# Optimization experiments

Hardware: AMD Instinct MI355X
Metric: run time of the kernel (lower is better)

Reference implementation:

```python
import jax, jax.numpy as jnp
import numpy as np

EMBED_DIM = 2048
NUM_HEADS = 16
NUM_KV_HEADS = 4
KEY_DIM = EMBED_DIM // NUM_HEADS  # 128
B, S = 2, 2048


def setup_inputs() -> dict:
    key = jax.random.key(0)
    ks = jax.random.split(key, 8)
    kv_dim = KEY_DIM * NUM_KV_HEADS
    sc_in = 1.0 / np.sqrt(EMBED_DIM)
    return {
        "query": jax.random.normal(ks[0], (B, S, EMBED_DIM), jnp.float32),
        "key": jax.random.normal(ks[1], (B, S, EMBED_DIM), jnp.float32),
        "value": jax.random.normal(ks[2], (B, S, EMBED_DIM), jnp.float32),
        "mask": jnp.ones((B, S), jnp.float32),
        "Wq": jax.random.normal(ks[3], (EMBED_DIM, EMBED_DIM), jnp.float32) * sc_in,
        "Wk": jax.random.normal(ks[4], (EMBED_DIM, kv_dim), jnp.float32) * sc_in,
        "Wv": jax.random.normal(ks[5], (EMBED_DIM, kv_dim), jnp.float32) * sc_in,
        "Wo": jax.random.normal(ks[6], (EMBED_DIM, EMBED_DIM), jnp.float32) * sc_in,
    }


def reference(query, key, value, mask, Wq, Wk, Wv, Wo):
    b, sq, _ = query.shape
    skv = key.shape[1]
    scale = 1.0 / float(KEY_DIM) ** 0.5
    # projections (no bias)
    q = (query @ Wq).reshape(b, sq, NUM_HEADS, KEY_DIM).transpose(0, 2, 1, 3)      # [B,H,Sq,D]
    k = (key @ Wk).reshape(b, skv, NUM_KV_HEADS, KEY_DIM).transpose(0, 2, 1, 3)    # [B,Hkv,Skv,D]
    v = (value @ Wv).reshape(b, skv, NUM_KV_HEADS, KEY_DIM).transpose(0, 2, 1, 3)  # [B,Hkv,Skv,D]
    n_rep = NUM_HEADS // NUM_KV_HEADS
    k_rep = jnp.repeat(k, n_rep, axis=1)  # [B,H,Skv,D]
    v_rep = jnp.repeat(v, n_rep, axis=1)  # [B,H,Skv,D]
    scores = jnp.einsum("bhqd,bhkd->bhqk", q, k_rep) * scale  # [B,H,Sq,Skv]
    scores = scores + (1.0 - mask[:, None, None, :].astype(scores.dtype)) * -1e9
    attn = jax.nn.softmax(scores, axis=-1)
    out = jnp.einsum("bhqk,bhkd->bhqd", attn, v_rep)  # [B,H,Sq,D]
    out = out.transpose(0, 2, 1, 3).reshape(b, sq, EMBED_DIM)
    return out @ Wo
```

## Files before the change

### kernel.cpp

```cpp
#include <hip/hip_runtime.h>
#include <hip/hip_bf16.h>

#define B_    2
#define S_    2048
#define E_    2048
#define H_    16
#define HKV_  4
#define D_    128
#define NTOK  4096
#define KVDIM 512

typedef __bf16 bf16x8 __attribute__((ext_vector_type(8)));
typedef __bf16 bf16x4 __attribute__((ext_vector_type(4)));
typedef float  f32x4  __attribute__((ext_vector_type(4)));

__device__ __forceinline__ void async_copy16(const void* g, void* l) {
  __builtin_amdgcn_global_load_lds(
      (const __attribute__((address_space(1))) unsigned int*)g,
      (__attribute__((address_space(3))) unsigned int*)l, 16, 0, 0);
}

__global__ __launch_bounds__(256) void transpose_all(
    const float* __restrict__ Wq, const float* __restrict__ Wk,
    const float* __restrict__ Wv, const float* __restrict__ Wo,
    __bf16* __restrict__ WTq, __bf16* __restrict__ WTk,
    __bf16* __restrict__ WTv, __bf16* __restrict__ WoT) {
  const float* in;
  __bf16* out;
  int C;
  switch (blockIdx.z) {
    case 0:  in = Wq; out = WTq; C = E_;   break;
    case 1:  in = Wk; out = WTk; C = KVDIM; break;
    case 2:  in = Wv; out = WTv; C = KVDIM; break;
    default: in = Wo; out = WoT; C = E_;   break;
  }
  const int c0 = blockIdx.x * 32;
  if (c0 >= C) return;
  const int r0 = blockIdx.y * 32;
  __shared__ float t[32][33];
  const int tr = threadIdx.x >> 3;
  const int tc = (threadIdx.x & 7) * 4;
  const float* ip = in + (size_t)(r0 + tr) * C + c0 + tc;
#pragma unroll
  for (int i = 0; i < 4; ++i) t[tr][tc + i] = ip[i];
  __syncthreads();
  __bf16* op = out + (size_t)(c0 + tr) * E_ + r0 + tc;
#pragma unroll
  for (int i = 0; i < 4; ++i) op[i] = (__bf16)t[tc + i][tr];
}

__global__ __launch_bounds__(256) void convert_q(const float* __restrict__ in,
                                                 __bf16* __restrict__ ob) {
  const size_t i = ((size_t)blockIdx.x * 256 + threadIdx.x) * 8;
  const f32x4 a0 = *(const f32x4*)(in + i);
  const f32x4 a1 = *(const f32x4*)(in + i + 4);
  bf16x8 v;
#pragma unroll
  for (int j = 0; j < 4; ++j) { v[j] = (__bf16)a0[j]; v[4 + j] = (__bf16)a1[j]; }
  *(bf16x8*)(ob + i) = v;
}

__global__ __launch_bounds__(512, 1) void gemm_pipe(
    const __bf16* __restrict__ A, const __bf16* __restrict__ Bt,
    float* __restrict__ Cf, __bf16* __restrict__ Cb, int M, int N, int K,
    int epi) {
  __shared__ __align__(16) __bf16 lds[2 * 24576];

  const int n0 = blockIdx.x * 256;
  const int m0 = blockIdx.y * 128;
  const int tid = threadIdx.x;
  const int w = tid >> 6;
  const int lane = tid & 63;
  const int quad = lane >> 4;
  const int l16 = lane & 15;
  const int wm = w >> 2;
  const int wn = w & 3;
  const int lr = lane >> 3;
  const int ls = lane & 7;

  const __bf16* pa[2];
  const __bf16* pb[4];
#pragma unroll
  for (int r = 0; r < 2; ++r) {
    const int row = r * 64 + w * 8 + lr;
    pa[r] = A + (size_t)(m0 + row) * K + ((ls ^ (row & 7)) * 8);
  }
#pragma unroll
  for (int r = 0; r < 4; ++r) {
    const int row = r * 64 + w * 8 + lr;
    pb[r] = Bt + (size_t)(n0 + row) * K + ((ls ^ (row & 7)) * 8);
  }

  auto stageA = [&](int bufi) {
    __bf16* base = lds + bufi * 24576;
#pragma unroll
    for (int r = 0; r < 2; ++r) {
      async_copy16(pa[r], base + (size_t)(r * 64 + w * 8) * 64);
      pa[r] += 64;
    }
  };
  auto stageB = [&](int bufi) {
    __bf16* base = lds + bufi * 24576 + 8192;
#pragma unroll
    for (int r = 0; r < 4; ++r) {
      async_copy16(pb[r], base + (size_t)(r * 64 + w * 8) * 64);
      pb[r] += 64;
    }
  };

  f32x4 acc[4][4] = {};
  const int NT = K >> 6;
  const int xr = l16 & 7;

  stageA(0);
  stageB(0);
  stageB(1);
  asm volatile("s_waitcnt vmcnt(4)" ::: "memory");
  __builtin_amdgcn_s_barrier();

  for (int t = 0; t < NT; ++t) {
    const __bf16* lA = lds + (t & 1) * 24576;
    const __bf16* lB = lA + 8192;

    bf16x8 af[2][2], bfr[4][2];
#pragma unroll
    for (int f = 0; f < 2; ++f) {
      const int rowb = (wm * 64 + f * 16 + l16) * 64;
#pragma unroll
      for (int ks = 0; ks < 2; ++ks)
        af[f][ks] = *(const bf16x8*)&lA[rowb + (((ks * 4 + quad) ^ xr) * 8)];
    }
#pragma unroll
    for (int g = 0; g < 4; ++g) {
      const int rowb = (wn * 64 + g * 16 + l16) * 64;
#pragma unroll
      for (int ks = 0; ks < 2; ++ks)
        bfr[g][ks] = *(const bf16x8*)&lB[rowb + (((ks * 4 + quad) ^ xr) * 8)];
    }
    if (t + 1 < NT) stageA((t + 1) & 1);
    __builtin_amdgcn_s_barrier();
    asm volatile("s_waitcnt lgkmcnt(0)" ::: "memory");
    __builtin_amdgcn_sched_barrier(0);
    __builtin_amdgcn_s_setprio(1);
#pragma unroll
    for (int f = 0; f < 2; ++f)
#pragma unroll
      for (int g = 0; g < 4; ++g) {
        acc[f][g] = __builtin_amdgcn_mfma_f32_16x16x32_bf16(af[f][0], bfr[g][0],
                                                            acc[f][g], 0, 0, 0);
        acc[f][g] = __builtin_amdgcn_mfma_f32_16x16x32_bf16(af[f][1], bfr[g][1],
                                                            acc[f][g], 0, 0, 0);
      }
    __builtin_amdgcn_s_setprio(0);
    __builtin_amdgcn_s_barrier();

    bf16x8 ah[2][2];
#pragma unroll
    for (int f = 0; f < 2; ++f) {
      const int rowb = (wm * 64 + (f + 2) * 16 + l16) * 64;
#pragma unroll
      for (int ks = 0; ks < 2; ++ks)
        ah[f][ks] = *(const bf16x8*)&lA[rowb + (((ks * 4 + quad) ^ xr) * 8)];
    }
    if (t + 2 < NT) stageB(t & 1);
    __builtin_amdgcn_s_barrier();
    asm volatile("s_waitcnt lgkmcnt(0)" ::: "memory");
    __builtin_amdgcn_sched_barrier(0);
    __builtin_amdgcn_s_setprio(1);
#pragma unroll
    for (int f = 0; f < 2; ++f)
#pragma unroll
      for (int g = 0; g < 4; ++g) {
        acc[f + 2][g] = __builtin_amdgcn_mfma_f32_16x16x32_bf16(
            ah[f][0], bfr[g][0], acc[f + 2][g], 0, 0, 0);
        acc[f + 2][g] = __builtin_amdgcn_mfma_f32_16x16x32_bf16(
            ah[f][1], bfr[g][1], acc[f + 2][g], 0, 0, 0);
      }
    __builtin_amdgcn_s_setprio(0);

    if (t + 2 < NT) {
      asm volatile("s_waitcnt vmcnt(4)" ::: "memory");
      __builtin_amdgcn_s_barrier();
    } else if (t + 1 < NT) {
      asm volatile("s_waitcnt vmcnt(0)" ::: "memory");
      __builtin_amdgcn_s_barrier();
    }
  }

#pragma unroll
  for (int f = 0; f < 4; ++f) {
#pragma unroll
    for (int g = 0; g < 4; ++g) {
#pragma unroll
      for (int r = 0; r < 4; ++r) {
        const int m = m0 + wm * 64 + f * 16 + quad * 4 + r;
        const int n = n0 + wn * 64 + g * 16 + l16;
        if (epi == 0) Cf[(size_t)m * N + n] = acc[f][g][r];
        else          Cb[(size_t)m * N + n] = (__bf16)acc[f][g][r];
      }
    }
  }
}

__global__ __launch_bounds__(256, 2) void gemm_kv(
    const float* __restrict__ key, const float* __restrict__ value,
    const __bf16* __restrict__ WTk, const __bf16* __restrict__ WTv,
    __bf16* __restrict__ Kp, __bf16* __restrict__ Vt) {
  __shared__ __align__(16) __bf16 As[128 * 32];
  __shared__ __align__(16) __bf16 Bs[128 * 32];

  const int bx = blockIdx.x;
  const float* A;
  const __bf16* Bt;
  int n0, epi;
  if (bx < 4) { A = key;   Bt = WTk; n0 = bx * 128;       epi = 0; }
  else        { A = value; Bt = WTv; n0 = (bx - 4) * 128; epi = 1; }
  const int m0 = blockIdx.y * 128;
  const int K = E_;
  const int N = KVDIM;

  const int tid = threadIdx.x;
  const int w = tid >> 6;
  const int lane = tid & 63;
  const int quad = lane >> 4;
  const int l16 = lane & 15;
  const int wr = w >> 1, wc = w & 1;
  const int brow = lane >> 2;
  const int bcol = (lane & 3) * 8;
  const int arow = lane >> 2;
  const int acol = (lane & 3) * 8;

  f32x4 acc[4][4] = {};

  for (int k0 = 0; k0 < K; k0 += 32) {
    __syncthreads();
#pragma unroll
    for (int c = 0; c < 2; ++c) {
      const int chunk = w * 2 + c;
      const int row = chunk * 16 + brow;
      async_copy16(Bt + (size_t)(n0 + row) * K + k0 + bcol, &Bs[chunk * 512]);
    }
#pragma unroll
    for (int s = 0; s < 2; ++s) {
      const int row = w * 32 + s * 16 + arow;
      const float* src = A + (size_t)(m0 + row) * K + k0 + acol;
      const f32x4 a0 = *(const f32x4*)src;
      const f32x4 a1 = *(const f32x4*)(src + 4);
      bf16x8 v;
#pragma unroll
      for (int j = 0; j < 4; ++j) { v[j] = (__bf16)a0[j]; v[4 + j] = (__bf16)a1[j]; }
      *(bf16x8*)&As[row * 32 + acol] = v;
    }
    __syncthreads();
    bf16x8 af[4], bfr[4];
#pragma unroll
    for (int i = 0; i < 4; ++i)
      af[i] = *(const bf16x8*)&As[(wr * 64 + i * 16 + l16) * 32 + quad * 8];
#pragma unroll
    for (int j = 0; j < 4; ++j)
      bfr[j] = *(const bf16x8*)&Bs[(wc * 64 + j * 16 + l16) * 32 + quad * 8];
#pragma unroll
    for (int i = 0; i < 4; ++i)
#pragma unroll
      for (int j = 0; j < 4; ++j)
        acc[i][j] = __builtin_amdgcn_mfma_f32_16x16x32_bf16(af[i], bfr[j],
                                                            acc[i][j], 0, 0, 0);
  }

#pragma unroll
  for (int i = 0; i < 4; ++i) {
#pragma unroll
    for (int j = 0; j < 4; ++j) {
#pragma unroll
      for (int r = 0; r < 4; ++r) {
        const int m = m0 + wr * 64 + i * 16 + quad * 4 + r;
        const int n = n0 + wc * 64 + j * 16 + l16;
        if (epi == 0) {
          Kp[(size_t)m * N + n] = (__bf16)acc[i][j][r];
        } else {
          const int b = m >> 11, s = m & (S_ - 1);
          Vt[((size_t)((b * HKV_ + (n >> 7)) * D_ + (n & (D_ - 1)))) * S_ + s] =
              (__bf16)acc[i][j][r];
        }
      }
    }
  }
}

__global__ __launch_bounds__(256, 2) void attn_kernel(
    const __bf16* __restrict__ Q, const __bf16* __restrict__ Kp,
    const __bf16* __restrict__ Vt, const float* __restrict__ mask,
    __bf16* __restrict__ Oa) {
  __shared__ __align__(16) __bf16 K_lds[64][136];
  __shared__ __align__(16) __bf16 V_lds[128][72];
  __shared__ __align__(16) __bf16 P_lds[4][32][72];

  const int tid = threadIdx.x;
  const int w = tid >> 6, lane = tid & 63, quad = lane >> 4, l16 = lane & 15;
  const int bh = blockIdx.y;
  const int b = bh >> 4, h = bh & 15, hkv = h >> 2;
  const int q0 = blockIdx.x * 128 + w * 32;

  const __bf16* qbase = Q + (size_t)(b * S_ + q0) * E_ + h * D_;
  bf16x8 qf[2][4];
#pragma unroll
  for (int m = 0; m < 2; ++m)
#pragma unroll
    for (int ks = 0; ks < 4; ++ks)
      qf[m][ks] = *(const bf16x8*)(qbase + (size_t)(m * 16 + l16) * E_ +
                                   ks * 32 + quad * 8);

  const __bf16* kbase = Kp + (size_t)(b * S_) * KVDIM + hkv * D_;
  const __bf16* vbase = Vt + (size_t)((b * HKV_ + hkv) * D_) * S_;
  const float* mbase = mask + b * S_;

  f32x4 o[2][8] = {};
  f32x4 lsum[2] = {};
  const float scale = 0.08838834764831845f;

  for (int kt = 0; kt < S_; kt += 64) {
    __syncthreads();
#pragma unroll
    for (int i = 0; i < 4; ++i) {
      const int r = w * 16 + i * 4 + (lane >> 4);
      bf16x8 kv = *(const bf16x8*)(kbase + (size_t)(kt + r) * KVDIM +
                                   (lane & 15) * 8);
      *(bf16x8*)&K_lds[r][(lane & 15) * 8] = kv;
    }
#pragma unroll
    for (int i = 0; i < 4; ++i) {
      const int r = w * 32 + i * 8 + (lane >> 3);
      bf16x8 vv = *(const bf16x8*)(vbase + (size_t)r * S_ + kt +
                                   (lane & 7) * 8);
      *(bf16x8*)&V_lds[r][(lane & 7) * 8] = vv;
    }
    __syncthreads();

    f32x4 s[2][4] = {};
    __builtin_amdgcn_s_setprio(1);
#pragma unroll
    for (int ks = 0; ks < 4; ++ks) {
#pragma unroll
      for (int n = 0; n < 4; ++n) {
        bf16x8 kf = *(const bf16x8*)&K_lds[n * 16 + l16][ks * 32 + quad * 8];
        s[0][n] = __builtin_amdgcn_mfma_f32_16x16x32_bf16(qf[0][ks], kf,
                                                          s[0][n], 0, 0, 0);
        s[1][n] = __builtin_amdgcn_mfma_f32_16x16x32_bf16(qf[1][ks], kf,
                                                          s[1][n], 0, 0, 0);
      }
    }
    __builtin_amdgcn_s_setprio(0);

    float bias[4];
#pragma unroll
    for (int n = 0; n < 4; ++n)
      bias[n] = (1.0f - mbase[kt + n * 16 + l16]) * -1e9f;
#pragma unroll
    for (int m = 0; m < 2; ++m) {
#pragma unroll
      for (int n = 0; n < 4; ++n) {
#pragma unroll
        for (int r = 0; r < 4; ++r) {
          const float p = __expf(s[m][n][r] * scale + bias[n]);
          lsum[m][r] += p;
          P_lds[w][m * 16 + quad * 4 + r][n * 16 + l16] = (__bf16)p;
        }
      }
    }

    __builtin_amdgcn_s_setprio(1);
#pragma unroll
    for (int ks2 = 0; ks2 < 2; ++ks2) {
      bf16x8 pa[2];
#pragma unroll
      for (int m = 0; m < 2; ++m)
        pa[m] = *(const bf16x8*)&P_lds[w][m * 16 + l16][ks2 * 32 + quad * 8];
#pragma unroll
      for (int dt = 0; dt < 8; ++dt) {
        bf16x8 vf = *(const bf16x8*)&V_lds[dt * 16 + l16][ks2 * 32 + quad * 8];
        o[0][dt] = __builtin_amdgcn_mfma_f32_16x16x32_bf16(pa[0], vf,
                                                           o[0][dt], 0, 0, 0);
        o[1][dt] = __builtin_amdgcn_mfma_f32_16x16x32_bf16(pa[1], vf,
                                                           o[1][dt], 0, 0, 0);
      }
    }
    __builtin_amdgcn_s_setprio(0);
  }

  __bf16* obase = Oa + (size_t)(b * S_ + q0) * E_ + h * D_;
#pragma unroll
  for (int m = 0; m < 2; ++m) {
#pragma unroll
    for (int r = 0; r < 4; ++r) {
      float v = lsum[m][r];
#pragma unroll
      for (int off = 1; off < 16; off <<= 1) v += __shfl_xor(v, off);
      const float inv = 1.0f / v;
#pragma unroll
      for (int dt = 0; dt < 8; ++dt)
        obase[(size_t)(m * 16 + quad * 4 + r) * E_ + dt * 16 + l16] =
            (__bf16)(o[m][dt][r] * inv);
    }
  }
}

extern "C" void kernel_launch(void* const* d_in, const int* in_sizes, int n_in,
                              void* d_out, int out_size, void* d_ws,
                              size_t ws_size, hipStream_t stream) {
  const float* query = (const float*)d_in[0];
  const float* key   = (const float*)d_in[1];
  const float* value = (const float*)d_in[2];
  const float* mask  = (const float*)d_in[3];
  const float* Wq    = (const float*)d_in[4];
  const float* Wk    = (const float*)d_in[5];
  const float* Wv    = (const float*)d_in[6];
  const float* Wo    = (const float*)d_in[7];
  float* out = (float*)d_out;

  __bf16* ws   = (__bf16*)d_ws;
  __bf16* Qp   = ws;
  __bf16* Kp   = Qp + (size_t)NTOK * E_;
  __bf16* Vt   = Kp + (size_t)NTOK * KVDIM;
  __bf16* WoT  = Vt + (size_t)NTOK * KVDIM;
  __bf16* WTq  = WoT + (size_t)E_ * E_;
  __bf16* WTk  = WTq + (size_t)E_ * E_;
  __bf16* WTv  = WTk + (size_t)KVDIM * E_;
  __bf16* Attn = WTq;
  __bf16* qb   = (__bf16*)d_out;

  transpose_all<<<dim3(64, 64, 4), 256, 0, stream>>>(Wq, Wk, Wv, Wo,
                                                     WTq, WTk, WTv, WoT);
  convert_q<<<dim3(4096), 256, 0, stream>>>(query, qb);
  gemm_kv<<<dim3(8, 32), 256, 0, stream>>>(key, value, WTk, WTv, Kp, Vt);
  gemm_pipe<<<dim3(E_ / 256, NTOK / 128), 512, 0, stream>>>(
      qb, WTq, nullptr, Qp, NTOK, E_, E_, 1);
  attn_kernel<<<dim3(S_ / 128, B_ * H_), 256, 0, stream>>>(Qp, Kp, Vt, mask,
                                                           Attn);
  gemm_pipe<<<dim3(E_ / 256, NTOK / 128), 512, 0, stream>>>(
      Attn, WoT, out, nullptr, NTOK, E_, E_, 0);
}
```

Before: 411.2 us.

## Fuse query conversion into transpose, swizzle GEMM tiles, keep attention P in registers

Query fp32-to-bf16 conversion now runs as an extra z-slice of the weight transpose kernel, which drops one launch, and the transpose uses wider 64-row tiles with vectorized loads and stores. The projection GEMM remaps block indices with a swizzle to improve L2 reuse across tiles. The attention kernel computes S transposed (K as the A operand), turns the probabilities into the PV operand layout with lane shuffles instead of a round trip through LDS, loads the mask bias as vectors, and raises occupancy to 3 blocks per SM. The risks are more shuffle instructions and higher register pressure under the tighter launch bound.

```diff
diff --git a/kernel.cpp b/kernel.cpp
--- a/kernel.cpp
+++ b/kernel.cpp
@@ -24,7 +24,25 @@
     const float* __restrict__ Wq, const float* __restrict__ Wk,
     const float* __restrict__ Wv, const float* __restrict__ Wo,
     __bf16* __restrict__ WTq, __bf16* __restrict__ WTk,
-    __bf16* __restrict__ WTv, __bf16* __restrict__ WoT) {
+    __bf16* __restrict__ WTv, __bf16* __restrict__ WoT,
+    const float* __restrict__ query, __bf16* __restrict__ qb) {
+  if (blockIdx.z == 4) {
+    const size_t i =
+        (((size_t)blockIdx.y * 64 + blockIdx.x) * 256 + threadIdx.x) * 16;
+    const f32x4 a0 = *(const f32x4*)(query + i);
+    const f32x4 a1 = *(const f32x4*)(query + i + 4);
+    const f32x4 a2 = *(const f32x4*)(query + i + 8);
+    const f32x4 a3 = *(const f32x4*)(query + i + 12);
+    bf16x8 v0, v1;
+#pragma unroll
+    for (int j = 0; j < 4; ++j) {
+      v0[j] = (__bf16)a0[j]; v0[4 + j] = (__bf16)a1[j];
+      v1[j] = (__bf16)a2[j]; v1[4 + j] = (__bf16)a3[j];
+    }
+    *(bf16x8*)(qb + i) = v0;
+    *(bf16x8*)(qb + i + 8) = v1;
+    return;
+  }
   const float* in;
   __bf16* out;
   int C;
@@ -36,28 +54,24 @@
   }
   const int c0 = blockIdx.x * 32;
   if (c0 >= C) return;
-  const int r0 = blockIdx.y * 32;
-  __shared__ float t[32][33];
-  const int tr = threadIdx.x >> 3;
-  const int tc = (threadIdx.x & 7) * 4;
-  const float* ip = in + (size_t)(r0 + tr) * C + c0 + tc;
-#pragma unroll
-  for (int i = 0; i < 4; ++i) t[tr][tc + i] = ip[i];
+  const int r0 = blockIdx.y * 64;
+  __shared__ float t[32][65];
+  const int lr = threadIdx.x >> 2;
+  const int lc = (threadIdx.x & 3) * 8;
+  const float* ip = in + (size_t)(r0 + lr) * C + c0 + lc;
+  const f32x4 a0 = *(const f32x4*)ip;
+  const f32x4 a1 = *(const f32x4*)(ip + 4);
+#pragma unroll
+  for (int j = 0; j < 4; ++j) t[lc + j][lr] = a0[j];
+#pragma unroll
+  for (int j = 0; j < 4; ++j) t[lc + 4 + j][lr] = a1[j];
   __syncthreads();
-  __bf16* op = out + (size_t)(c0 + tr) * E_ + r0 + tc;
-#pragma unroll
-  for (int i = 0; i < 4; ++i) op[i] = (__bf16)t[tc + i][tr];
-}
-
-__global__ __launch_bounds__(256) void convert_q(const float* __restrict__ in,
-                                                 __bf16* __restrict__ ob) {
-  const size_t i = ((size_t)blockIdx.x * 256 + threadIdx.x) * 8;
-  const f32x4 a0 = *(const f32x4*)(in + i);
-  const f32x4 a1 = *(const f32x4*)(in + i + 4);
+  const int oc = threadIdx.x >> 3;
+  const int orr = (threadIdx.x & 7) * 8;
   bf16x8 v;
 #pragma unroll
-  for (int j = 0; j < 4; ++j) { v[j] = (__bf16)a0[j]; v[4 + j] = (__bf16)a1[j]; }
-  *(bf16x8*)(ob + i) = v;
+  for (int j = 0; j < 8; ++j) v[j] = (__bf16)t[oc][orr + j];
+  *(bf16x8*)(out + (size_t)(c0 + oc) * E_ + r0 + orr) = v;
 }
 
 __global__ __launch_bounds__(512, 1) void gemm_pipe(
@@ -66,8 +80,10 @@
     int epi) {
   __shared__ __align__(16) __bf16 lds[2 * 24576];
 
-  const int n0 = blockIdx.x * 256;
-  const int m0 = blockIdx.y * 128;
+  const int lin = blockIdx.y * gridDim.x + blockIdx.x;
+  const int swz = (lin & 7) * 32 + (lin >> 3);
+  const int n0 = (swz >> 5) * 256;
+  const int m0 = (swz & 31) * 128;
   const int tid = threadIdx.x;
   const int w = tid >> 6;
   const int lane = tid & 63;
@@ -287,13 +303,12 @@
   }
 }
 
-__global__ __launch_bounds__(256, 2) void attn_kernel(
+__global__ __launch_bounds__(256, 3) void attn_kernel(
     const __bf16* __restrict__ Q, const __bf16* __restrict__ Kp,
     const __bf16* __restrict__ Vt, const float* __restrict__ mask,
     __bf16* __restrict__ Oa) {
   __shared__ __align__(16) __bf16 K_lds[64][136];
   __shared__ __align__(16) __bf16 V_lds[128][72];
-  __shared__ __align__(16) __bf16 P_lds[4][32][72];
 
   const int tid = threadIdx.x;
   const int w = tid >> 6, lane = tid & 63, quad = lane >> 4, l16 = lane & 15;
@@ -315,8 +330,11 @@
   const float* mbase = mask + b * S_;
 
   f32x4 o[2][8] = {};
-  f32x4 lsum[2] = {};
+  float lsum[2] = {0.0f, 0.0f};
   const float scale = 0.08838834764831845f;
+  const bool oddq = (quad & 1) != 0;
+  const bool hig = (quad >> 1) != 0;
+  const bool sw = hig != oddq;
 
   for (int kt = 0; kt < S_; kt += 64) {
     __syncthreads();
@@ -336,51 +354,77 @@
     }
     __syncthreads();
 
-    f32x4 s[2][4] = {};
+    f32x4 breg[4];
+#pragma unroll
+    for (int n = 0; n < 4; ++n)
+      breg[n] = *(const f32x4*)(mbase + kt + n * 16 + quad * 4);
+
+    uint2 pb[2][4];
+#pragma unroll
+    for (int m = 0; m < 2; ++m) {
+      f32x4 st[4] = {};
+      __builtin_amdgcn_s_setprio(1);
+#pragma unroll
+      for (int ks = 0; ks < 4; ++ks) {
+#pragma unroll
+        for (int n = 0; n < 4; ++n) {
+          bf16x8 kf = *(const bf16x8*)&K_lds[n * 16 + l16][ks * 32 + quad * 8];
+          st[n] = __builtin_amdgcn_mfma_f32_16x16x32_bf16(kf, qf[m][ks],
+                                                          st[n], 0, 0, 0);
+        }
+      }
+      __builtin_amdgcn_s_setprio(0);
+#pragma unroll
+      for (int n = 0; n < 4; ++n) {
+        union { bf16x4 b; uint2 u; } t;
+#pragma unroll
+        for (int r = 0; r < 4; ++r) {
+          const float p =
+              __expf(st[n][r] * scale + (1.0f - breg[n][r]) * -1e9f);
+          lsum[m] += p;
+          t.b[r] = (__bf16)p;
+        }
+        pb[m][n] = t.u;
+      }
+    }
+
     __builtin_amdgcn_s_setprio(1);
 #pragma unroll
-    for (int ks = 0; ks < 4; ++ks) {
-#pragma unroll
-      for (int n = 0; n < 4; ++n) {
-        bf16x8 kf = *(const bf16x8*)&K_lds[n * 16 + l16][ks * 32 + quad * 8];
-        s[0][n] = __builtin_amdgcn_mfma_f32_16x16x32_bf16(qf[0][ks], kf,
-                                                          s[0][n], 0, 0, 0);
-        s[1][n] = __builtin_amdgcn_mfma_f32_16x16x32_bf16(qf[1][ks], kf,
-                                                          s[1][n], 0, 0, 0);
-      }
-    }
-    __builtin_amdgcn_s_setprio(0);
-
-    float bias[4];
-#pragma unroll
-    for (int n = 0; n < 4; ++n)
-      bias[n] = (1.0f - mbase[kt + n * 16 + l16]) * -1e9f;
-#pragma unroll
-    for (int m = 0; m < 2; ++m) {
-#pragma unroll
-      for (int n = 0; n < 4; ++n) {
-#pragma unroll
-        for (int r = 0; r < 4; ++r) {
-          const float p = __expf(s[m][n][r] * scale + bias[n]);
-          lsum[m][r] += p;
-          P_lds[w][m * 16 + quad * 4 + r][n * 16 + l16] = (__bf16)p;
-        }
-      }
-    }
-
-    __builtin_amdgcn_s_setprio(1);
-#pragma unroll
     for (int ks2 = 0; ks2 < 2; ++ks2) {
-      bf16x8 pa[2];
-#pragma unroll
-      for (int m = 0; m < 2; ++m)
-        pa[m] = *(const bf16x8*)&P_lds[w][m * 16 + l16][ks2 * 32 + quad * 8];
+      bf16x8 pav[2];
+#pragma unroll
+      for (int m = 0; m < 2; ++m) {
+        const uint2 plo = pb[m][2 * ks2];
+        const uint2 phi = pb[m][2 * ks2 + 1];
+        uint2 plo16, phi16;
+        plo16.x = __shfl_xor((int)plo.x, 16);
+        plo16.y = __shfl_xor((int)plo.y, 16);
+        phi16.x = __shfl_xor((int)phi.x, 16);
+        phi16.y = __shfl_xor((int)phi.y, 16);
+        const uint2 p0l = oddq ? plo16 : plo;
+        const uint2 p0h = oddq ? plo : plo16;
+        const uint2 p1l = oddq ? phi16 : phi;
+        const uint2 p1h = oddq ? phi : phi16;
+        uint2 zsl = hig ? p0l : p1l;
+        uint2 zsh = hig ? p0h : p1h;
+        uint2 zl, zh;
+        zl.x = __shfl_xor((int)zsl.x, 32);
+        zl.y = __shfl_xor((int)zsl.y, 32);
+        zh.x = __shfl_xor((int)zsh.x, 32);
+        zh.y = __shfl_xor((int)zsh.y, 32);
+        const uint2 kl = hig ? p1l : p0l;
+        const uint2 kh = hig ? p1h : p0h;
+        union { bf16x8 b; uint2 u[2]; } pa_u;
+        pa_u.u[0] = sw ? zl : kl;
+        pa_u.u[1] = sw ? zh : kh;
+        pav[m] = pa_u.b;
+      }
 #pragma unroll
       for (int dt = 0; dt < 8; ++dt) {
         bf16x8 vf = *(const bf16x8*)&V_lds[dt * 16 + l16][ks2 * 32 + quad * 8];
-        o[0][dt] = __builtin_amdgcn_mfma_f32_16x16x32_bf16(pa[0], vf,
+        o[0][dt] = __builtin_amdgcn_mfma_f32_16x16x32_bf16(pav[0], vf,
                                                            o[0][dt], 0, 0, 0);
-        o[1][dt] = __builtin_amdgcn_mfma_f32_16x16x32_bf16(pa[1], vf,
+        o[1][dt] = __builtin_amdgcn_mfma_f32_16x16x32_bf16(pav[1], vf,
                                                            o[1][dt], 0, 0, 0);
       }
     }
@@ -390,12 +434,13 @@
   __bf16* obase = Oa + (size_t)(b * S_ + q0) * E_ + h * D_;
 #pragma unroll
   for (int m = 0; m < 2; ++m) {
+    float tot = lsum[m];
+    tot += __shfl_xor(tot, 16);
+    tot += __shfl_xor(tot, 32);
 #pragma unroll
     for (int r = 0; r < 4; ++r) {
-      float v = lsum[m][r];
-#pragma unroll
-      for (int off = 1; off < 16; off <<= 1) v += __shfl_xor(v, off);
-      const float inv = 1.0f / v;
+      const float sr = __shfl(tot, (quad << 4) | (quad * 4 + r));
+      const float inv = 1.0f / sr;
 #pragma unroll
       for (int dt = 0; dt < 8; ++dt)
         obase[(size_t)(m * 16 + quad * 4 + r) * E_ + dt * 16 + l16] =
@@ -428,14 +473,14 @@
   __bf16* Attn = WTq;
   __bf16* qb   = (__bf16*)d_out;
 
-  transpose_all<<<dim3(64, 64, 4), 256, 0, stream>>>(Wq, Wk, Wv, Wo,
-                                                     WTq, WTk, WTv, WoT);
-  convert_q<<<dim3(4096), 256, 0, stream>>>(query, qb);
+  transpose_all<<<dim3(64, 32, 5), 256, 0, stream>>>(Wq, Wk, Wv, Wo,
+                                                     WTq, WTk, WTv, WoT,
+                                                     query, qb);
   gemm_kv<<<dim3(8, 32), 256, 0, stream>>>(key, value, WTk, WTv, Kp, Vt);
-  gemm_pipe<<<dim3(E_ / 256, NTOK / 128), 512, 0, stream>>>(
+  gemm_pipe<<<dim3(8, 32), 512, 0, stream>>>(
       qb, WTq, nullptr, Qp, NTOK, E_, E_, 1);
   attn_kernel<<<dim3(S_ / 128, B_ * H_), 256, 0, stream>>>(Qp, Kp, Vt, mask,
                                                            Attn);
-  gemm_pipe<<<dim3(E_ / 256, NTOK / 128), 512, 0, stream>>>(
+  gemm_pipe<<<dim3(8, 32), 512, 0, stream>>>(
       Attn, WoT, out, nullptr, NTOK, E_, E_, 0);
 }
```

Result: slower. 520.4 us (+26.6%).
